# Performance work log

Hardware: AMD Instinct MI355X
Metric: run time of the kernel (lower is better)

Reference implementation:

```python
import jax, jax.numpy as jnp
import numpy as np

D_K = 64

def setup_inputs() -> dict:
    key = jax.random.key(0)
    k1, k2, k3, k4 = jax.random.split(key, 4)
    B, H, S, D = 4, 16, 2048, D_K
    q = jax.random.normal(k1, (B, H, S, D), dtype=jnp.float32)
    k = jax.random.normal(k2, (B, H, D, S), dtype=jnp.float32)  # pre-transposed, as module expects
    v = jax.random.normal(k3, (B, H, S, D), dtype=jnp.float32)
    mask = jax.random.randint(k4, (B, 1, 1, S), 0, 2).astype(jnp.bool_)
    return {"q": q, "k": k, "v": v, "mask": mask}

def reference(q, k, v, mask):
    # scores: [B,H,S,S] = q @ k / sqrt(d_k); k is already [B,H,d_k,S]
    scale = 1.0 / jnp.sqrt(jnp.asarray(D_K, dtype=q.dtype))
    scores = jnp.einsum('bhsd,bhdt->bhst', q, k) * scale
    scores = jnp.where(mask, jnp.asarray(-1e9, dtype=scores.dtype), scores)
    attn = jax.nn.softmax(scores, axis=-1)
    context = jnp.einsum('bhst,bhtd->bhsd', attn, v)
    return (context, attn)
```

## Files before the change

### kernel.cpp

```cpp
#include <hip/hip_runtime.h>
#include <cstdint>

#define S_LEN 2048
#define D_K   64
#define M_Q   32
#define SSTR  2056
#define QSTR  72
#define CSTR  68
#define LOG2E 1.44269504088896340736f

typedef __attribute__((ext_vector_type(8))) short short8;
typedef __attribute__((ext_vector_type(4))) float f4;

__device__ __forceinline__ short f2b(float f) {
    union { float f; uint32_t u; } x; x.f = f;
    uint32_t r = x.u + 0x7FFFu + ((x.u >> 16) & 1u);
    return (short)(r >> 16);
}
__device__ __forceinline__ float b2f(short b) {
    union { uint32_t u; float f; } x;
    x.u = ((uint32_t)(uint16_t)b) << 16;
    return x.f;
}

__global__ __launch_bounds__(256, 1) void attn_fused(
    const float* __restrict__ qg, const float* __restrict__ kg,
    const float* __restrict__ vg, const int* __restrict__ mg,
    float* __restrict__ ctxg, float* __restrict__ attng)
{
    __shared__ short sS[M_Q * SSTR];
    __shared__ short sQ[M_Q * QSTR];
    __shared__ float sCtx[M_Q * CSTR];

    const int tid  = threadIdx.x;
    const int wave = tid >> 6;
    const int lane = tid & 63;
    const int quad = lane >> 4;
    const int l16  = lane & 15;

    const int bh = blockIdx.x >> 6;
    const int qt = blockIdx.x & 63;
    const int bb = bh >> 4;

    const float* qp = qg + (size_t)bh * S_LEN * D_K + (size_t)qt * M_Q * D_K;
    const float* kp = kg + (size_t)bh * D_K * S_LEN;
    const float* vp = vg + (size_t)bh * S_LEN * D_K;
    const int*   mp = mg + (size_t)bb * S_LEN;
    float* cp = ctxg + (size_t)bh * S_LEN * D_K + (size_t)qt * M_Q * D_K;
    float* ap = attng + ((size_t)bh * S_LEN + (size_t)qt * M_Q) * S_LEN;

    {
        const int r = tid >> 3;
        const int c = (tid & 7) * 8;
        f4 a0 = *(const f4*)(qp + r * D_K + c);
        f4 a1 = *(const f4*)(qp + r * D_K + c + 4);
        short8 s8;
        #pragma unroll
        for (int j = 0; j < 4; ++j) { s8[j] = f2b(a0[j]); s8[4 + j] = f2b(a1[j]); }
        *(short8*)(&sQ[r * QSTR + c]) = s8;
    }
    __syncthreads();

    short8 aq[2][2];
    #pragma unroll
    for (int rb = 0; rb < 2; ++rb)
        #pragma unroll
        for (int h = 0; h < 2; ++h)
            aq[rb][h] = *(const short8*)(&sQ[(rb * 16 + l16) * QSTR + h * 32 + quad * 8]);

    for (int cblk = 0; cblk < 32; ++cblk) {
        const int t  = (wave * 32 + cblk) * 16 + l16;
        const int mk = mp[t];
        short8 blo, bhi;
        #pragma unroll
        for (int j = 0; j < 8; ++j) {
            blo[j] = f2b(kp[(size_t)(quad * 8 + j) * S_LEN + t]);
            bhi[j] = f2b(kp[(size_t)(32 + quad * 8 + j) * S_LEN + t]);
        }
        #pragma unroll
        for (int rb = 0; rb < 2; ++rb) {
            f4 acc = {0.f, 0.f, 0.f, 0.f};
            acc = __builtin_amdgcn_mfma_f32_16x16x32_bf16(aq[rb][0], blo, acc, 0, 0, 0);
            acc = __builtin_amdgcn_mfma_f32_16x16x32_bf16(aq[rb][1], bhi, acc, 0, 0, 0);
            #pragma unroll
            for (int rr = 0; rr < 4; ++rr) {
                const int row = rb * 16 + quad * 4 + rr;
                const float val = mk ? -1e9f : acc[rr] * 0.125f;
                sS[row * SSTR + t] = f2b(val);
            }
        }
    }
    __syncthreads();

    {
        const int r = tid >> 3;
        const int i = tid & 7;
        short* srow = &sS[r * SSTR];
        float mx = -3.0e38f;
        for (int kk = 0; kk < 32; ++kk) {
            short8 x = *(const short8*)(srow + 8 * i + 64 * kk);
            #pragma unroll
            for (int j = 0; j < 8; ++j) mx = fmaxf(mx, b2f(x[j]));
        }
        mx = fmaxf(mx, __shfl_xor(mx, 1));
        mx = fmaxf(mx, __shfl_xor(mx, 2));
        mx = fmaxf(mx, __shfl_xor(mx, 4));
        float sum = 0.f;
        for (int kk = 0; kk < 32; ++kk) {
            short8 x = *(const short8*)(srow + 8 * i + 64 * kk);
            #pragma unroll
            for (int j = 0; j < 8; ++j)
                sum += __builtin_amdgcn_exp2f((b2f(x[j]) - mx) * LOG2E);
        }
        sum += __shfl_xor(sum, 1);
        sum += __shfl_xor(sum, 2);
        sum += __shfl_xor(sum, 4);
        const float inv = 1.0f / sum;
        float* arow = ap + (size_t)r * S_LEN;
        for (int kk = 0; kk < 32; ++kk) {
            const int c0 = 8 * i + 64 * kk;
            short8 x = *(const short8*)(srow + c0);
            short8 pb;
            f4 o0, o1;
            #pragma unroll
            for (int j = 0; j < 8; ++j) {
                const float e = __builtin_amdgcn_exp2f((b2f(x[j]) - mx) * LOG2E) * inv;
                pb[j] = f2b(e);
                if (j < 4) o0[j] = e; else o1[j - 4] = e;
            }
            *(short8*)(srow + c0) = pb;
            __builtin_nontemporal_store(o0, (f4*)(arow + c0));
            __builtin_nontemporal_store(o1, (f4*)(arow + c0 + 4));
        }
    }
    __syncthreads();

    f4 acc[2][4];
    #pragma unroll
    for (int rb = 0; rb < 2; ++rb)
        #pragma unroll
        for (int db = 0; db < 4; ++db)
            acc[rb][db] = (f4){0.f, 0.f, 0.f, 0.f};

    for (int ks = 0; ks < 16; ++ks) {
        const int t0 = wave * 512 + ks * 32;
        short8 a0 = *(const short8*)(&sS[l16 * SSTR + t0 + quad * 8]);
        short8 a1 = *(const short8*)(&sS[(16 + l16) * SSTR + t0 + quad * 8]);
        #pragma unroll
        for (int db = 0; db < 4; ++db) {
            short8 bv;
            #pragma unroll
            for (int j = 0; j < 8; ++j)
                bv[j] = f2b(vp[(size_t)(t0 + quad * 8 + j) * D_K + db * 16 + l16]);
            acc[0][db] = __builtin_amdgcn_mfma_f32_16x16x32_bf16(a0, bv, acc[0][db], 0, 0, 0);
            acc[1][db] = __builtin_amdgcn_mfma_f32_16x16x32_bf16(a1, bv, acc[1][db], 0, 0, 0);
        }
    }

    for (int w2 = 0; w2 < 4; ++w2) {
        if (wave == w2) {
            #pragma unroll
            for (int rb = 0; rb < 2; ++rb)
                #pragma unroll
                for (int db = 0; db < 4; ++db)
                    #pragma unroll
                    for (int rr = 0; rr < 4; ++rr) {
                        const int row = rb * 16 + quad * 4 + rr;
                        const int col = db * 16 + l16;
                        if (w2 == 0) sCtx[row * CSTR + col]  = acc[rb][db][rr];
                        else         sCtx[row * CSTR + col] += acc[rb][db][rr];
                    }
        }
        __syncthreads();
    }

    {
        const int r = tid >> 3;
        const int i = tid & 7;
        f4 o0 = *(const f4*)(&sCtx[r * CSTR + 8 * i]);
        f4 o1 = *(const f4*)(&sCtx[r * CSTR + 8 * i + 4]);
        *(f4*)(cp + (size_t)r * D_K + 8 * i)     = o0;
        *(f4*)(cp + (size_t)r * D_K + 8 * i + 4) = o1;
    }
}

extern "C" void kernel_launch(void* const* d_in, const int* in_sizes, int n_in,
                              void* d_out, int out_size, void* d_ws, size_t ws_size,
                              hipStream_t stream) {
    const float* q = (const float*)d_in[0];
    const float* k = (const float*)d_in[1];
    const float* v = (const float*)d_in[2];
    const int* mask = (const int*)d_in[3];
    float* out = (float*)d_out;
    float* ctx  = out;
    float* attn = out + (size_t)4 * 16 * 2048 * 64;
    attn_fused<<<dim3(4096), dim3(256), 0, stream>>>(q, k, v, mask, ctx, attn);
}
```

Baseline: 1.829 ms.

## Pre-transpose K/V to bf16 in workspace and halve query tile per block

Adds a pre-pass kernel that converts K and V to bf16 in the workspace and transposes them, so the attention kernel can fetch MFMA operands as contiguous 16-byte vector loads instead of strided scalar fp32 loads with per-element conversion. The query tile drops from 32 to 16 rows, which doubles the grid and allows two blocks per CU. The PV product is restructured so each wave owns a 16-column slice of the head dimension, which removes the cross-wave shared-memory reduction and its serialized barriers. The cost is two extra launches plus extra workspace traffic, and with the smaller tile each K/V tile is reused across fewer queries.

After: 1.539 ms. 1.19x faster.

```diff
diff --git a/kernel.cpp b/kernel.cpp
--- a/kernel.cpp
+++ b/kernel.cpp
@@ -3,10 +3,8 @@
 
 #define S_LEN 2048
 #define D_K   64
-#define M_Q   32
+#define M_Q   16
 #define SSTR  2056
-#define QSTR  72
-#define CSTR  68
 #define LOG2E 1.44269504088896340736f
 
 typedef __attribute__((ext_vector_type(8))) short short8;
@@ -23,14 +21,39 @@
     return x.f;
 }
 
-__global__ __launch_bounds__(256, 1) void attn_fused(
+__global__ __launch_bounds__(256) void transpose_cvt(
+    const float* __restrict__ in, short* __restrict__ out,
+    int inRS, int outRS, int tileAlongRow)
+{
+    __shared__ short T[64][72];
+    const int head = blockIdx.x >> 5;
+    const int tile = blockIdx.x & 31;
+    const int r0 = tileAlongRow ? tile * 64 : 0;
+    const int c0 = tileAlongRow ? 0 : tile * 64;
+    const size_t hoff = (size_t)head * S_LEN * D_K;
+    const int rr = threadIdx.x >> 2;
+    const int cc = (threadIdx.x & 3) * 16;
+    const float* ip = in + hoff + (size_t)(r0 + rr) * inRS + c0 + cc;
+    #pragma unroll
+    for (int j4 = 0; j4 < 4; ++j4) {
+        f4 x = *(const f4*)(ip + j4 * 4);
+        #pragma unroll
+        for (int j = 0; j < 4; ++j) T[cc + j4 * 4 + j][rr] = f2b(x[j]);
+    }
+    __syncthreads();
+    short* op = out + hoff + (size_t)(c0 + rr) * outRS + r0 + cc;
+    *(short8*)(op)     = *(const short8*)(&T[rr][cc]);
+    *(short8*)(op + 8) = *(const short8*)(&T[rr][cc + 8]);
+}
+
+template<bool BF16>
+__global__ __launch_bounds__(256, 2) void attn_fused(
     const float* __restrict__ qg, const float* __restrict__ kg,
-    const float* __restrict__ vg, const int* __restrict__ mg,
+    const float* __restrict__ vg, const short* __restrict__ kbg,
+    const short* __restrict__ vtg, const int* __restrict__ mg,
     float* __restrict__ ctxg, float* __restrict__ attng)
 {
     __shared__ short sS[M_Q * SSTR];
-    __shared__ short sQ[M_Q * QSTR];
-    __shared__ float sCtx[M_Q * CSTR];
 
     const int tid  = threadIdx.x;
     const int wave = tid >> 6;
@@ -38,76 +61,71 @@
     const int quad = lane >> 4;
     const int l16  = lane & 15;
 
-    const int bh = blockIdx.x >> 6;
-    const int qt = blockIdx.x & 63;
-    const int bb = bh >> 4;
+    const int bh = blockIdx.x >> 7;
+    const int qt = blockIdx.x & 127;
 
     const float* qp = qg + (size_t)bh * S_LEN * D_K + (size_t)qt * M_Q * D_K;
     const float* kp = kg + (size_t)bh * D_K * S_LEN;
     const float* vp = vg + (size_t)bh * S_LEN * D_K;
-    const int*   mp = mg + (size_t)bb * S_LEN;
+    const short* kb = kbg + (size_t)bh * S_LEN * D_K;
+    const short* vt = vtg + (size_t)bh * D_K * S_LEN;
+    const int*   mp = mg + (size_t)(bh >> 4) * S_LEN;
     float* cp = ctxg + (size_t)bh * S_LEN * D_K + (size_t)qt * M_Q * D_K;
     float* ap = attng + ((size_t)bh * S_LEN + (size_t)qt * M_Q) * S_LEN;
 
-    {
-        const int r = tid >> 3;
-        const int c = (tid & 7) * 8;
-        f4 a0 = *(const f4*)(qp + r * D_K + c);
-        f4 a1 = *(const f4*)(qp + r * D_K + c + 4);
-        short8 s8;
+    short8 aq[2];
+    #pragma unroll
+    for (int h = 0; h < 2; ++h) {
+        f4 x0 = *(const f4*)(qp + l16 * D_K + h * 32 + quad * 8);
+        f4 x1 = *(const f4*)(qp + l16 * D_K + h * 32 + quad * 8 + 4);
         #pragma unroll
-        for (int j = 0; j < 4; ++j) { s8[j] = f2b(a0[j]); s8[4 + j] = f2b(a1[j]); }
-        *(short8*)(&sQ[r * QSTR + c]) = s8;
-    }
-    __syncthreads();
-
-    short8 aq[2][2];
-    #pragma unroll
-    for (int rb = 0; rb < 2; ++rb)
-        #pragma unroll
-        for (int h = 0; h < 2; ++h)
-            aq[rb][h] = *(const short8*)(&sQ[(rb * 16 + l16) * QSTR + h * 32 + quad * 8]);
+        for (int j = 0; j < 4; ++j) { aq[h][j] = f2b(x0[j]); aq[h][4 + j] = f2b(x1[j]); }
+    }
 
     for (int cblk = 0; cblk < 32; ++cblk) {
-        const int t  = (wave * 32 + cblk) * 16 + l16;
+        const int t0 = (wave * 32 + cblk) * 16;
+        const int t  = t0 + l16;
         const int mk = mp[t];
         short8 blo, bhi;
+        if (BF16) {
+            blo = *(const short8*)(kb + (size_t)t * D_K + quad * 8);
+            bhi = *(const short8*)(kb + (size_t)t * D_K + 32 + quad * 8);
+        } else {
+            #pragma unroll
+            for (int j = 0; j < 8; ++j) {
+                blo[j] = f2b(kp[(size_t)(quad * 8 + j) * S_LEN + t]);
+                bhi[j] = f2b(kp[(size_t)(32 + quad * 8 + j) * S_LEN + t]);
+            }
+        }
+        f4 acc = {0.f, 0.f, 0.f, 0.f};
+        acc = __builtin_amdgcn_mfma_f32_16x16x32_bf16(aq[0], blo, acc, 0, 0, 0);
+        acc = __builtin_amdgcn_mfma_f32_16x16x32_bf16(aq[1], bhi, acc, 0, 0, 0);
         #pragma unroll
-        for (int j = 0; j < 8; ++j) {
-            blo[j] = f2b(kp[(size_t)(quad * 8 + j) * S_LEN + t]);
-            bhi[j] = f2b(kp[(size_t)(32 + quad * 8 + j) * S_LEN + t]);
-        }
-        #pragma unroll
-        for (int rb = 0; rb < 2; ++rb) {
-            f4 acc = {0.f, 0.f, 0.f, 0.f};
-            acc = __builtin_amdgcn_mfma_f32_16x16x32_bf16(aq[rb][0], blo, acc, 0, 0, 0);
-            acc = __builtin_amdgcn_mfma_f32_16x16x32_bf16(aq[rb][1], bhi, acc, 0, 0, 0);
-            #pragma unroll
-            for (int rr = 0; rr < 4; ++rr) {
-                const int row = rb * 16 + quad * 4 + rr;
-                const float val = mk ? -1e9f : acc[rr] * 0.125f;
-                sS[row * SSTR + t] = f2b(val);
-            }
+        for (int rr = 0; rr < 4; ++rr) {
+            const int row = quad * 4 + rr;
+            const float val = mk ? -1e9f : acc[rr] * 0.125f;
+            sS[row * SSTR + t] = f2b(val);
         }
     }
     __syncthreads();
 
     {
-        const int r = tid >> 3;
-        const int i = tid & 7;
+        const int r = tid >> 4;
+        const int i = tid & 15;
         short* srow = &sS[r * SSTR];
         float mx = -3.0e38f;
-        for (int kk = 0; kk < 32; ++kk) {
-            short8 x = *(const short8*)(srow + 8 * i + 64 * kk);
+        for (int kk = 0; kk < 16; ++kk) {
+            short8 x = *(const short8*)(srow + 8 * i + 128 * kk);
             #pragma unroll
             for (int j = 0; j < 8; ++j) mx = fmaxf(mx, b2f(x[j]));
         }
         mx = fmaxf(mx, __shfl_xor(mx, 1));
         mx = fmaxf(mx, __shfl_xor(mx, 2));
         mx = fmaxf(mx, __shfl_xor(mx, 4));
+        mx = fmaxf(mx, __shfl_xor(mx, 8));
         float sum = 0.f;
-        for (int kk = 0; kk < 32; ++kk) {
-            short8 x = *(const short8*)(srow + 8 * i + 64 * kk);
+        for (int kk = 0; kk < 16; ++kk) {
+            short8 x = *(const short8*)(srow + 8 * i + 128 * kk);
             #pragma unroll
             for (int j = 0; j < 8; ++j)
                 sum += __builtin_amdgcn_exp2f((b2f(x[j]) - mx) * LOG2E);
@@ -115,10 +133,11 @@
         sum += __shfl_xor(sum, 1);
         sum += __shfl_xor(sum, 2);
         sum += __shfl_xor(sum, 4);
+        sum += __shfl_xor(sum, 8);
         const float inv = 1.0f / sum;
         float* arow = ap + (size_t)r * S_LEN;
-        for (int kk = 0; kk < 32; ++kk) {
-            const int c0 = 8 * i + 64 * kk;
+        for (int kk = 0; kk < 16; ++kk) {
+            const int c0 = 8 * i + 128 * kk;
             short8 x = *(const short8*)(srow + c0);
             short8 pb;
             f4 o0, o1;
@@ -135,53 +154,24 @@
     }
     __syncthreads();
 
-    f4 acc[2][4];
+    f4 o = {0.f, 0.f, 0.f, 0.f};
+    const int d = wave * 16 + l16;
+    for (int ks = 0; ks < 64; ++ks) {
+        const int t0 = ks * 32;
+        short8 a = *(const short8*)(&sS[l16 * SSTR + t0 + quad * 8]);
+        short8 bv;
+        if (BF16) {
+            bv = *(const short8*)(vt + (size_t)d * S_LEN + t0 + quad * 8);
+        } else {
+            #pragma unroll
+            for (int j = 0; j < 8; ++j)
+                bv[j] = f2b(vp[(size_t)(t0 + quad * 8 + j) * D_K + d]);
+        }
+        o = __builtin_amdgcn_mfma_f32_16x16x32_bf16(a, bv, o, 0, 0, 0);
+    }
     #pragma unroll
-    for (int rb = 0; rb < 2; ++rb)
-        #pragma unroll
-        for (int db = 0; db < 4; ++db)
-            acc[rb][db] = (f4){0.f, 0.f, 0.f, 0.f};
-
-    for (int ks = 0; ks < 16; ++ks) {
-        const int t0 = wave * 512 + ks * 32;
-        short8 a0 = *(const short8*)(&sS[l16 * SSTR + t0 + quad * 8]);
-        short8 a1 = *(const short8*)(&sS[(16 + l16) * SSTR + t0 + quad * 8]);
-        #pragma unroll
-        for (int db = 0; db < 4; ++db) {
-            short8 bv;
-            #pragma unroll
-            for (int j = 0; j < 8; ++j)
-                bv[j] = f2b(vp[(size_t)(t0 + quad * 8 + j) * D_K + db * 16 + l16]);
-            acc[0][db] = __builtin_amdgcn_mfma_f32_16x16x32_bf16(a0, bv, acc[0][db], 0, 0, 0);
-            acc[1][db] = __builtin_amdgcn_mfma_f32_16x16x32_bf16(a1, bv, acc[1][db], 0, 0, 0);
-        }
-    }
-
-    for (int w2 = 0; w2 < 4; ++w2) {
-        if (wave == w2) {
-            #pragma unroll
-            for (int rb = 0; rb < 2; ++rb)
-                #pragma unroll
-                for (int db = 0; db < 4; ++db)
-                    #pragma unroll
-                    for (int rr = 0; rr < 4; ++rr) {
-                        const int row = rb * 16 + quad * 4 + rr;
-                        const int col = db * 16 + l16;
-                        if (w2 == 0) sCtx[row * CSTR + col]  = acc[rb][db][rr];
-                        else         sCtx[row * CSTR + col] += acc[rb][db][rr];
-                    }
-        }
-        __syncthreads();
-    }
-
-    {
-        const int r = tid >> 3;
-        const int i = tid & 7;
-        f4 o0 = *(const f4*)(&sCtx[r * CSTR + 8 * i]);
-        f4 o1 = *(const f4*)(&sCtx[r * CSTR + 8 * i + 4]);
-        *(f4*)(cp + (size_t)r * D_K + 8 * i)     = o0;
-        *(f4*)(cp + (size_t)r * D_K + 8 * i + 4) = o1;
-    }
+    for (int rr = 0; rr < 4; ++rr)
+        cp[(size_t)(quad * 4 + rr) * D_K + d] = o[rr];
 }
 
 extern "C" void kernel_launch(void* const* d_in, const int* in_sizes, int n_in,
@@ -194,5 +184,17 @@
     float* out = (float*)d_out;
     float* ctx  = out;
     float* attn = out + (size_t)4 * 16 * 2048 * 64;
-    attn_fused<<<dim3(4096), dim3(256), 0, stream>>>(q, k, v, mask, ctx, attn);
-}
+
+    const size_t KV_ELEMS = (size_t)4 * 16 * 2048 * 64;
+    const size_t WS_NEED  = KV_ELEMS * 2 * sizeof(short);
+
+    if (d_ws && ws_size >= WS_NEED) {
+        short* kb = (short*)d_ws;
+        short* vt = kb + KV_ELEMS;
+        transpose_cvt<<<dim3(2048), dim3(256), 0, stream>>>(k, kb, S_LEN, D_K, 0);
+        transpose_cvt<<<dim3(2048), dim3(256), 0, stream>>>(v, vt, D_K, S_LEN, 1);
+        attn_fused<true><<<dim3(8192), dim3(256), 0, stream>>>(q, k, v, kb, vt, mask, ctx, attn);
+    } else {
+        attn_fused<false><<<dim3(8192), dim3(256), 0, stream>>>(q, k, v, nullptr, nullptr, mask, ctx, attn);
+    }
+}
```
